# Kernel tuning notes

Measured on AMD Instinct MI355X. Metric: run time of the kernel, lower is better.

Reference implementation:

```python
import jax, jax.numpy as jnp
import numpy as np

D_MODEL = 1024
N_HEADS = 16
D_HEAD = D_MODEL // N_HEADS  # 64
SCALE = 1.0 / float(np.sqrt(D_HEAD))


def setup_inputs() -> dict:
    key = jax.random.key(0)
    kx, kq, kk, kv, ko = jax.random.split(key, 5)
    B, L = 1, 4096
    x = jax.random.normal(kx, (B, L, D_MODEL), dtype=jnp.float32)
    init = 0.02  # small init so softmax isn't saturated
    Wq = jax.random.normal(kq, (D_MODEL, D_MODEL), dtype=jnp.float32) * init
    Wk = jax.random.normal(kk, (D_MODEL, D_MODEL), dtype=jnp.float32) * init
    Wv = jax.random.normal(kv, (D_MODEL, D_MODEL), dtype=jnp.float32) * init
    Wo = jax.random.normal(ko, (D_MODEL, D_MODEL), dtype=jnp.float32) * init
    return {"x": x, "Wq": Wq, "Wk": Wk, "Wv": Wv, "Wo": Wo}


def reference(x, Wq, Wk, Wv, Wo):
    # x: [B, L, d_model]; torch Linear (no bias): y = x @ W.T
    B, L, _ = x.shape

    def split_heads(t):  # [B, L, d_model] -> [B, H, L, Dh]
        return t.reshape(B, L, N_HEADS, D_HEAD).transpose(0, 2, 1, 3)

    q = split_heads(x @ Wq.T)
    k = split_heads(x @ Wk.T)
    v = split_heads(x @ Wv.T)

    # Full (non-flash) attention: explicit [B, H, L, L] scores (causal=False, eval dropout=0)
    scores = jnp.einsum("bhld,bhmd->bhlm", q, k) * SCALE
    attn = jax.nn.softmax(scores, axis=-1)
    out = jnp.einsum("bhlm,bhmd->bhld", attn, v)

    out = out.transpose(0, 2, 1, 3).reshape(B, L, D_MODEL)
    return out @ Wo.T
```

## Files before the change

### kernel.cpp

```cpp
#include <hip/hip_runtime.h>

typedef _Float16 f16_t;
typedef __fp16 fp16x2 __attribute__((ext_vector_type(2)));
typedef _Float16 f16x2 __attribute__((ext_vector_type(2)));
typedef _Float16 f16x4 __attribute__((ext_vector_type(4)));
typedef _Float16 f16x8 __attribute__((ext_vector_type(8)));
typedef float f32x4 __attribute__((ext_vector_type(4)));

#define D_MODEL 1024
#define LSEQ 4096
#define NH 16
#define DH 64
#define QSCALE 0.18033688011112042f

#define GLDS16(g, l)                                                     \
    __builtin_amdgcn_global_load_lds(                                    \
        (const __attribute__((address_space(1))) void*)(g),              \
        (__attribute__((address_space(3))) void*)(l), 16, 0, 0)

#define WAIT_VM(n) asm volatile("s_waitcnt vmcnt(" #n ")" ::: "memory")

__global__ __launch_bounds__(256) void cvt_all(const float* __restrict__ x,
                                               const float* __restrict__ w0,
                                               const float* __restrict__ w1,
                                               const float* __restrict__ w2,
                                               const float* __restrict__ w3,
                                               f16_t* __restrict__ xb,
                                               f16_t* __restrict__ wq) {
    const int id = blockIdx.x;
    const float* src;
    f16_t* dst;
    float scale = 1.f;
    int i;
    if (id < 4096) {
        src = x; dst = xb;
        i = (id * 256 + threadIdx.x) * 4;
    } else {
        const int r = id - 4096;
        const int q = r >> 10;
        src = (q == 0) ? w0 : (q == 1) ? w1 : (q == 2) ? w2 : w3;
        if (q == 0) scale = QSCALE;
        dst = wq + (size_t)q * (D_MODEL * D_MODEL);
        i = ((r & 1023) * 256 + threadIdx.x) * 4;
    }
    float4 v = *(const float4*)&src[i];
    alignas(8) f16_t o4[4] = {(f16_t)(v.x * scale), (f16_t)(v.y * scale),
                              (f16_t)(v.z * scale), (f16_t)(v.w * scale)};
    *(uint2*)&dst[i] = *(const uint2*)o4;
}

__global__ __launch_bounds__(256, 3) void gemm_f16(const f16_t* __restrict__ A,
                                                   const f16_t* __restrict__ B,
                                                   void* __restrict__ Cout,
                                                   f16_t* __restrict__ v4out,
                                                   int M, int N, int K, int mode) {
    __shared__ alignas(16) f16_t sm[24576];

    const int tid  = threadIdx.x;
    const int wave = tid >> 6;
    const int lane = tid & 63;
    const int quad = lane >> 4;
    const int l16  = lane & 15;
    const int wm = (wave & 1) * 64;
    const int wn = (wave >> 1) * 64;

    const int gx  = gridDim.x;
    const int gy  = gridDim.y;
    const int lid = blockIdx.y * gx + blockIdx.x;
    const int xcd = lid & 7;
    const int sub = lid >> 3;
    const int bm  = (xcd * (gx >> 3) + sub / gy) * 128;
    const int bn  = (sub % gy) * 128;

    f32x4 acc[4][4] = {};
    const int nk = K / 32;

    auto stage = [&](int kt, int b) {
        const int c0 = wave * 2;
        GLDS16(&A[(size_t)(bm + c0 * 16 + l16) * K + kt * 32 + quad * 8],
               &sm[b * 4096 + c0 * 512]);
        GLDS16(&A[(size_t)(bm + (c0 + 1) * 16 + l16) * K + kt * 32 + quad * 8],
               &sm[b * 4096 + (c0 + 1) * 512]);
        GLDS16(&B[(size_t)(bn + c0 * 16 + l16) * K + kt * 32 + quad * 8],
               &sm[12288 + b * 4096 + c0 * 512]);
        GLDS16(&B[(size_t)(bn + (c0 + 1) * 16 + l16) * K + kt * 32 + quad * 8],
               &sm[12288 + b * 4096 + (c0 + 1) * 512]);
    };

    stage(0, 0);
    stage(1, 1);
    for (int kt = 0; kt < nk; ++kt) {
        const int cb = kt % 3;
        if (kt < nk - 1) WAIT_VM(4);
        else             WAIT_VM(0);
        __syncthreads();
        if (kt + 2 < nk) stage(kt + 2, (kt + 2) % 3);

        f16x8 af[4], bfr[4];
#pragma unroll
        for (int mt = 0; mt < 4; ++mt)
            af[mt] = *(const f16x8*)&sm[cb * 4096 + ((wm >> 4) + mt) * 512 + lane * 8];
#pragma unroll
        for (int nt = 0; nt < 4; ++nt)
            bfr[nt] = *(const f16x8*)&sm[12288 + cb * 4096 + ((wn >> 4) + nt) * 512 + lane * 8];
#pragma unroll
        for (int mt = 0; mt < 4; ++mt)
#pragma unroll
            for (int nt = 0; nt < 4; ++nt)
                acc[mt][nt] = __builtin_amdgcn_mfma_f32_16x16x32_f16(
                    bfr[nt], af[mt], acc[mt][nt], 0, 0, 0);
    }

    const bool isV = (mode == 0) && (bn >= 2 * D_MODEL);
    if (!isV) {
#pragma unroll
        for (int mt = 0; mt < 4; ++mt)
#pragma unroll
            for (int nt = 0; nt < 4; ++nt) {
                int row = bm + wm + mt * 16 + l16;
                int col = bn + wn + nt * 16 + quad * 4;
                if (mode == 0) {
                    f16x4 p = {(f16_t)acc[mt][nt][0], (f16_t)acc[mt][nt][1],
                               (f16_t)acc[mt][nt][2], (f16_t)acc[mt][nt][3]};
                    *(f16x4*)&((f16_t*)Cout)[((size_t)(col >> 6) * M + row) * 64 +
                                             (col & 63)] = p;
                } else {
                    *(f32x4*)&((float*)Cout)[(size_t)row * N + col] = acc[mt][nt];
                }
            }
    } else {
        __syncthreads();
#pragma unroll
        for (int mt = 0; mt < 4; ++mt)
#pragma unroll
            for (int nt = 0; nt < 4; ++nt) {
                f16x4 p = {(f16_t)acc[mt][nt][0], (f16_t)acc[mt][nt][1],
                           (f16_t)acc[mt][nt][2], (f16_t)acc[mt][nt][3]};
                *(f16x4*)&sm[(wm + mt * 16 + l16) * 136 + wn + nt * 16 + quad * 4] = p;
            }
        __syncthreads();
        const int hh = wave >> 1, lt = wave & 1;
        const int head = ((bn - 2 * D_MODEL) >> 6) + hh;
        const int ltg  = (bm >> 6) + lt;
        const int g = lane >> 4, l16f = lane & 15;
        f16_t* dst = v4out + (size_t)head * (LSEQ * DH) + (size_t)ltg * 4096;
#pragma unroll
        for (int c8 = 0; c8 < 8; ++c8) {
            const int mtp = c8 >> 2, dt = c8 & 3;
            alignas(16) f16_t buf[8];
#pragma unroll
            for (int j = 0; j < 8; ++j) {
                int key = lt * 64 + mtp * 32 + (j < 4 ? 4 * g + j : 16 + 4 * g + (j - 4));
                buf[j] = sm[key * 136 + hh * 64 + dt * 16 + l16f];
            }
            *(uint4*)&dst[c8 * 512 + lane * 8] = *(const uint4*)buf;
        }
    }
}

__global__ __launch_bounds__(512, 2) void gemm_wo(const f16_t* __restrict__ A,
                                                  const f16_t* __restrict__ B,
                                                  float* __restrict__ outF) {
    __shared__ alignas(16) f16_t sm[24576];

    const int tid  = threadIdx.x;
    const int wave = tid >> 6;
    const int lane = tid & 63;
    const int quad = lane >> 4;
    const int l16  = lane & 15;
    const int wm = (wave & 1) * 64;
    const int wn = (wave >> 1) * 32;
    const int bm = blockIdx.x * 128;
    const int bn = blockIdx.y * 128;
    const int K = D_MODEL;

    f32x4 acc[4][2] = {};
    const int nk = K / 32;

    auto stage = [&](int kt, int b) {
        f16_t* base = sm + b * 8192;
        GLDS16(&A[(size_t)(bm + wave * 16 + l16) * K + kt * 32 + quad * 8],
               &base[wave * 512]);
        GLDS16(&B[(size_t)(bn + wave * 16 + l16) * K + kt * 32 + quad * 8],
               &base[4096 + wave * 512]);
    };

    stage(0, 0);
    stage(1, 1);
    for (int kt = 0; kt < nk; ++kt) {
        const int cb = kt % 3;
        if (kt < nk - 1) WAIT_VM(2);
        else             WAIT_VM(0);
        __syncthreads();
        if (kt + 2 < nk) stage(kt + 2, (kt + 2) % 3);

        f16x8 af[4], bfr[2];
#pragma unroll
        for (int mt = 0; mt < 4; ++mt)
            af[mt] = *(const f16x8*)&sm[cb * 8192 + ((wm >> 4) + mt) * 512 + lane * 8];
#pragma unroll
        for (int nt = 0; nt < 2; ++nt)
            bfr[nt] = *(const f16x8*)&sm[cb * 8192 + 4096 + ((wn >> 4) + nt) * 512 + lane * 8];
#pragma unroll
        for (int mt = 0; mt < 4; ++mt)
#pragma unroll
            for (int nt = 0; nt < 2; ++nt)
                acc[mt][nt] = __builtin_amdgcn_mfma_f32_16x16x32_f16(
                    bfr[nt], af[mt], acc[mt][nt], 0, 0, 0);
    }

#pragma unroll
    for (int mt = 0; mt < 4; ++mt)
#pragma unroll
        for (int nt = 0; nt < 2; ++nt) {
            int row = bm + wm + mt * 16 + l16;
            int col = bn + wn + nt * 16 + quad * 4;
            *(f32x4*)&outF[(size_t)row * D_MODEL + col] = acc[mt][nt];
        }
}

__global__ __launch_bounds__(512, 4) void attn_kernel(const f16_t* __restrict__ qh,
                                                      const f16_t* __restrict__ kh,
                                                      const f16_t* __restrict__ v4,
                                                      f16_t* __restrict__ ao) {
    __shared__ alignas(16) f16_t smem[32768];
    __shared__ alignas(16) float lscr[8 * 64];
    f16_t* KsB = smem;
    f16_t* VsB = smem + 16384;

    const int tid  = threadIdx.x;
    const int wave = tid >> 6;
    const int lane = tid & 63;
    const int quad = lane >> 4;
    const int l16  = lane & 15;
    const int wq   = wave & 3;
    const int kha  = wave >> 2;

    const int id = blockIdx.x;
    const int head = id & 15;
    const int qrow0 = (id >> 4) * 128 + wq * 32;

    const f16_t* Q  = qh + (size_t)head * LSEQ * DH;
    const f16_t* K  = kh + (size_t)head * LSEQ * DH;
    const f16_t* V4 = v4 + (size_t)head * (LSEQ * DH);

    f16x8 qf[2][2];
#pragma unroll
    for (int qt = 0; qt < 2; ++qt)
#pragma unroll
        for (int kc = 0; kc < 2; ++kc)
            qf[qt][kc] = *(const f16x8*)
                &Q[(size_t)(qrow0 + qt * 16 + l16) * DH + kc * 32 + quad * 8];

    f32x4 o[4][2] = {};
    float lp[2] = {0.f, 0.f};

    auto stage = [&](int kt, int b) {
        f16_t* ks = KsB + (kha * 2 + b) * 4096;
        f16_t* vs = VsB + (kha * 2 + b) * 4096;
        const int ktg = kha * 32 + kt;
#pragma unroll
        for (int jj = 0; jj < 2; ++jj) {
            const int j = wq * 2 + jj;
            GLDS16(&K[(size_t)(ktg * 64 + wq * 16 + l16) * DH + jj * 32 + quad * 8],
                   &ks[j * 512]);
            GLDS16(&V4[(size_t)ktg * 4096 + wq * 1024 + jj * 512 + lane * 8],
                   &vs[wq * 1024 + jj * 512]);
        }
    };

    const int NT = LSEQ / 2 / 64;
    stage(0, 0);
    for (int kt = 0; kt < NT; ++kt) {
        const int cb = kt & 1;
        WAIT_VM(0);
        __syncthreads();
        if (kt + 1 < NT) stage(kt + 1, cb ^ 1);

        const f16_t* ks = KsB + (kha * 2 + cb) * 4096;
        const f16_t* vs = VsB + (kha * 2 + cb) * 4096;

        f32x4 sA[2][2] = {};
        {
            f16x8 kfA[4];
#pragma unroll
            for (int c = 0; c < 4; ++c)
                kfA[c] = *(const f16x8*)&ks[c * 512 + lane * 8];
#pragma unroll
            for (int h = 0; h < 2; ++h)
#pragma unroll
                for (int qt = 0; qt < 2; ++qt) {
                    sA[h][qt] = __builtin_amdgcn_mfma_f32_16x16x32_f16(
                        kfA[h * 2 + 0], qf[qt][0], sA[h][qt], 0, 0, 0);
                    sA[h][qt] = __builtin_amdgcn_mfma_f32_16x16x32_f16(
                        kfA[h * 2 + 1], qf[qt][1], sA[h][qt], 0, 0, 0);
                }
        }
        f32x4 sB[2][2] = {};
        {
            f16x8 kfB[4];
#pragma unroll
            for (int c = 0; c < 4; ++c)
                kfB[c] = *(const f16x8*)&ks[(4 + c) * 512 + lane * 8];
#pragma unroll
            for (int h = 0; h < 2; ++h)
#pragma unroll
                for (int qt = 0; qt < 2; ++qt) {
                    sB[h][qt] = __builtin_amdgcn_mfma_f32_16x16x32_f16(
                        kfB[h * 2 + 0], qf[qt][0], sB[h][qt], 0, 0, 0);
                    sB[h][qt] = __builtin_amdgcn_mfma_f32_16x16x32_f16(
                        kfB[h * 2 + 1], qf[qt][1], sB[h][qt], 0, 0, 0);
                }
        }

#pragma unroll
        for (int mtp = 0; mtp < 2; ++mtp) {
            f32x4 (*s)[2] = (mtp == 0) ? sA : sB;

            f16x8 vfd[4];
#pragma unroll
            for (int dt = 0; dt < 4; ++dt)
                vfd[dt] = *(const f16x8*)&vs[(mtp * 4 + dt) * 512 + lane * 8];

#pragma unroll
            for (int qt = 0; qt < 2; ++qt) {
                float e0 = __builtin_amdgcn_exp2f(s[0][qt][0]);
                float e1 = __builtin_amdgcn_exp2f(s[0][qt][1]);
                float e2 = __builtin_amdgcn_exp2f(s[0][qt][2]);
                float e3 = __builtin_amdgcn_exp2f(s[0][qt][3]);
                float e4 = __builtin_amdgcn_exp2f(s[1][qt][0]);
                float e5 = __builtin_amdgcn_exp2f(s[1][qt][1]);
                float e6 = __builtin_amdgcn_exp2f(s[1][qt][2]);
                float e7 = __builtin_amdgcn_exp2f(s[1][qt][3]);
                lp[qt] += ((e0 + e1) + (e2 + e3)) + ((e4 + e5) + (e6 + e7));
                fp16x2 p01 = __builtin_amdgcn_cvt_pkrtz(e0, e1);
                fp16x2 p23 = __builtin_amdgcn_cvt_pkrtz(e2, e3);
                fp16x2 p45 = __builtin_amdgcn_cvt_pkrtz(e4, e5);
                fp16x2 p67 = __builtin_amdgcn_cvt_pkrtz(e6, e7);
                f16x8 p = {__builtin_bit_cast(f16x2, p01)[0],
                           __builtin_bit_cast(f16x2, p01)[1],
                           __builtin_bit_cast(f16x2, p23)[0],
                           __builtin_bit_cast(f16x2, p23)[1],
                           __builtin_bit_cast(f16x2, p45)[0],
                           __builtin_bit_cast(f16x2, p45)[1],
                           __builtin_bit_cast(f16x2, p67)[0],
                           __builtin_bit_cast(f16x2, p67)[1]};
#pragma unroll
                for (int dt = 0; dt < 4; ++dt)
                    o[dt][qt] = __builtin_amdgcn_mfma_f32_16x16x32_f16(
                        vfd[dt], p, o[dt][qt], 0, 0, 0);
            }
        }
    }

    __syncthreads();
    float* scr = (float*)smem;
    if (wave >= 4) {
#pragma unroll
        for (int dt = 0; dt < 4; ++dt)
#pragma unroll
            for (int qt = 0; qt < 2; ++qt)
                *(f32x4*)&scr[(((wave - 4) * 8 + dt * 2 + qt) * 64 + lane) * 4] =
                    o[dt][qt];
#pragma unroll
        for (int qt = 0; qt < 2; ++qt)
            lscr[((wave - 4) * 2 + qt) * 64 + lane] = lp[qt];
    }
    __syncthreads();
    if (wave < 4) {
#pragma unroll
        for (int dt = 0; dt < 4; ++dt)
#pragma unroll
            for (int qt = 0; qt < 2; ++qt)
                o[dt][qt] += *(const f32x4*)
                    &scr[((wave * 8 + dt * 2 + qt) * 64 + lane) * 4];
#pragma unroll
        for (int qt = 0; qt < 2; ++qt) {
            float t = lp[qt] + lscr[(wave * 2 + qt) * 64 + lane];
            t += __shfl_xor(t, 16, 64);
            t += __shfl_xor(t, 32, 64);
            lp[qt] = 1.f / t;
        }
#pragma unroll
        for (int dt = 0; dt < 4; ++dt)
#pragma unroll
            for (int qt = 0; qt < 2; ++qt) {
                f16x4 ov = {(f16_t)(o[dt][qt][0] * lp[qt]),
                            (f16_t)(o[dt][qt][1] * lp[qt]),
                            (f16_t)(o[dt][qt][2] * lp[qt]),
                            (f16_t)(o[dt][qt][3] * lp[qt])};
                int qrow = qrow0 + qt * 16 + l16;
                *(f16x4*)&ao[(size_t)qrow * D_MODEL + head * 64 + dt * 16 +
                             quad * 4] = ov;
            }
    }
}

extern "C" void kernel_launch(void* const* d_in, const int* in_sizes, int n_in,
                              void* d_out, int out_size, void* d_ws, size_t ws_size,
                              hipStream_t stream) {
    const float* x  = (const float*)d_in[0];
    const float* Wq = (const float*)d_in[1];
    const float* Wk = (const float*)d_in[2];
    const float* Wv = (const float*)d_in[3];
    const float* Wo = (const float*)d_in[4];

    f16_t* xb = (f16_t*)d_ws;
    f16_t* wq = xb + (size_t)LSEQ * D_MODEL;
    f16_t* wo = wq + (size_t)3 * D_MODEL * D_MODEL;
    f16_t* qh = wo + (size_t)D_MODEL * D_MODEL;
    f16_t* kh = qh + (size_t)LSEQ * D_MODEL;
    f16_t* vh = kh + (size_t)LSEQ * D_MODEL;
    f16_t* v4 = vh + (size_t)LSEQ * D_MODEL;
    f16_t* ao = v4 + (size_t)LSEQ * D_MODEL;

    cvt_all<<<4096 + 4 * 1024, 256, 0, stream>>>(x, Wq, Wk, Wv, Wo, xb, wq);

    gemm_f16<<<dim3(LSEQ / 128, 3 * D_MODEL / 128), 256, 0, stream>>>(
        xb, wq, qh, v4, LSEQ, 3 * D_MODEL, D_MODEL, 0);

    attn_kernel<<<dim3((LSEQ / 128) * NH), 512, 0, stream>>>(qh, kh, v4, ao);

    gemm_wo<<<dim3(LSEQ / 128, D_MODEL / 128), 512, 0, stream>>>(
        ao, wo, (float*)d_out);
}
```

Baseline: 230.0 us.

## Fuse attention and output projection into one kernel with per-row-group counters

After: 266.8 us. 16.0% more time.

```diff
diff --git a/kernel.cpp b/kernel.cpp
--- a/kernel.cpp
+++ b/kernel.cpp
@@ -26,8 +26,10 @@
                                                const float* __restrict__ w2,
                                                const float* __restrict__ w3,
                                                f16_t* __restrict__ xb,
-                                               f16_t* __restrict__ wq) {
+                                               f16_t* __restrict__ wq,
+                                               unsigned int* __restrict__ cnt) {
     const int id = blockIdx.x;
+    if (id == 0 && threadIdx.x < 32) cnt[threadIdx.x] = 0;
     const float* src;
     f16_t* dst;
     float scale = 1.f;
@@ -158,240 +160,250 @@
     }
 }
 
-__global__ __launch_bounds__(512, 2) void gemm_wo(const f16_t* __restrict__ A,
-                                                  const f16_t* __restrict__ B,
-                                                  float* __restrict__ outF) {
-    __shared__ alignas(16) f16_t sm[24576];
+__global__ __launch_bounds__(512, 4) void attn_wo(
+        const f16_t* __restrict__ qh, const f16_t* __restrict__ kh,
+        const f16_t* __restrict__ v4, f16_t* __restrict__ ao,
+        const f16_t* __restrict__ wo, float* __restrict__ outF,
+        unsigned int* __restrict__ cnt) {
+    __shared__ alignas(16) f16_t smem[32768];
+    __shared__ alignas(16) float lscr[8 * 64];
 
     const int tid  = threadIdx.x;
     const int wave = tid >> 6;
     const int lane = tid & 63;
     const int quad = lane >> 4;
     const int l16  = lane & 15;
-    const int wm = (wave & 1) * 64;
-    const int wn = (wave >> 1) * 32;
-    const int bm = blockIdx.x * 128;
-    const int bn = blockIdx.y * 128;
-    const int K = D_MODEL;
-
-    f32x4 acc[4][2] = {};
-    const int nk = K / 32;
-
-    auto stage = [&](int kt, int b) {
-        f16_t* base = sm + b * 8192;
-        GLDS16(&A[(size_t)(bm + wave * 16 + l16) * K + kt * 32 + quad * 8],
-               &base[wave * 512]);
-        GLDS16(&B[(size_t)(bn + wave * 16 + l16) * K + kt * 32 + quad * 8],
-               &base[4096 + wave * 512]);
-    };
-
-    stage(0, 0);
-    stage(1, 1);
-    for (int kt = 0; kt < nk; ++kt) {
-        const int cb = kt % 3;
-        if (kt < nk - 1) WAIT_VM(2);
-        else             WAIT_VM(0);
-        __syncthreads();
-        if (kt + 2 < nk) stage(kt + 2, (kt + 2) % 3);
-
-        f16x8 af[4], bfr[2];
+
+    if (blockIdx.x < 512) {
+        f16_t* KsB = smem;
+        f16_t* VsB = smem + 16384;
+        const int wq  = wave & 3;
+        const int kha = wave >> 2;
+
+        const int id = blockIdx.x;
+        const int head = id & 15;
+        const int qrow0 = (id >> 4) * 128 + wq * 32;
+
+        const f16_t* Q  = qh + (size_t)head * LSEQ * DH;
+        const f16_t* K  = kh + (size_t)head * LSEQ * DH;
+        const f16_t* V4 = v4 + (size_t)head * (LSEQ * DH);
+
+        f16x8 qf[2][2];
+#pragma unroll
+        for (int qt = 0; qt < 2; ++qt)
+#pragma unroll
+            for (int kc = 0; kc < 2; ++kc)
+                qf[qt][kc] = *(const f16x8*)
+                    &Q[(size_t)(qrow0 + qt * 16 + l16) * DH + kc * 32 + quad * 8];
+
+        f32x4 o[4][2] = {};
+        float lp[2] = {0.f, 0.f};
+
+        auto stage = [&](int kt, int b) {
+            f16_t* ks = KsB + (kha * 2 + b) * 4096;
+            f16_t* vs = VsB + (kha * 2 + b) * 4096;
+            const int ktg = kha * 32 + kt;
+#pragma unroll
+            for (int jj = 0; jj < 2; ++jj) {
+                const int j = wq * 2 + jj;
+                GLDS16(&K[(size_t)(ktg * 64 + wq * 16 + l16) * DH + jj * 32 + quad * 8],
+                       &ks[j * 512]);
+                GLDS16(&V4[(size_t)ktg * 4096 + wq * 1024 + jj * 512 + lane * 8],
+                       &vs[wq * 1024 + jj * 512]);
+            }
+        };
+
+        const int NT = LSEQ / 2 / 64;
+        stage(0, 0);
+        for (int kt = 0; kt < NT; ++kt) {
+            const int cb = kt & 1;
+            WAIT_VM(0);
+            __syncthreads();
+            if (kt + 1 < NT) stage(kt + 1, cb ^ 1);
+
+            const f16_t* ks = KsB + (kha * 2 + cb) * 4096;
+            const f16_t* vs = VsB + (kha * 2 + cb) * 4096;
+
+            f32x4 sA[2][2] = {};
+            {
+                f16x8 kfA[4];
+#pragma unroll
+                for (int c = 0; c < 4; ++c)
+                    kfA[c] = *(const f16x8*)&ks[c * 512 + lane * 8];
+#pragma unroll
+                for (int h = 0; h < 2; ++h)
+#pragma unroll
+                    for (int qt = 0; qt < 2; ++qt) {
+                        sA[h][qt] = __builtin_amdgcn_mfma_f32_16x16x32_f16(
+                            kfA[h * 2 + 0], qf[qt][0], sA[h][qt], 0, 0, 0);
+                        sA[h][qt] = __builtin_amdgcn_mfma_f32_16x16x32_f16(
+                            kfA[h * 2 + 1], qf[qt][1], sA[h][qt], 0, 0, 0);
+                    }
+            }
+            f32x4 sB[2][2] = {};
+            {
+                f16x8 kfB[4];
+#pragma unroll
+                for (int c = 0; c < 4; ++c)
+                    kfB[c] = *(const f16x8*)&ks[(4 + c) * 512 + lane * 8];
+#pragma unroll
+                for (int h = 0; h < 2; ++h)
+#pragma unroll
+                    for (int qt = 0; qt < 2; ++qt) {
+                        sB[h][qt] = __builtin_amdgcn_mfma_f32_16x16x32_f16(
+                            kfB[h * 2 + 0], qf[qt][0], sB[h][qt], 0, 0, 0);
+                        sB[h][qt] = __builtin_amdgcn_mfma_f32_16x16x32_f16(
+                            kfB[h * 2 + 1], qf[qt][1], sB[h][qt], 0, 0, 0);
+                    }
+            }
+
+#pragma unroll
+            for (int mtp = 0; mtp < 2; ++mtp) {
+                f32x4 (*s)[2] = (mtp == 0) ? sA : sB;
+
+                f16x8 vfd[4];
+#pragma unroll
+                for (int dt = 0; dt < 4; ++dt)
+                    vfd[dt] = *(const f16x8*)&vs[(mtp * 4 + dt) * 512 + lane * 8];
+
+#pragma unroll
+                for (int qt = 0; qt < 2; ++qt) {
+                    float e0 = __builtin_amdgcn_exp2f(s[0][qt][0]);
+                    float e1 = __builtin_amdgcn_exp2f(s[0][qt][1]);
+                    float e2 = __builtin_amdgcn_exp2f(s[0][qt][2]);
+                    float e3 = __builtin_amdgcn_exp2f(s[0][qt][3]);
+                    float e4 = __builtin_amdgcn_exp2f(s[1][qt][0]);
+                    float e5 = __builtin_amdgcn_exp2f(s[1][qt][1]);
+                    float e6 = __builtin_amdgcn_exp2f(s[1][qt][2]);
+                    float e7 = __builtin_amdgcn_exp2f(s[1][qt][3]);
+                    lp[qt] += ((e0 + e1) + (e2 + e3)) + ((e4 + e5) + (e6 + e7));
+                    fp16x2 p01 = __builtin_amdgcn_cvt_pkrtz(e0, e1);
+                    fp16x2 p23 = __builtin_amdgcn_cvt_pkrtz(e2, e3);
+                    fp16x2 p45 = __builtin_amdgcn_cvt_pkrtz(e4, e5);
+                    fp16x2 p67 = __builtin_amdgcn_cvt_pkrtz(e6, e7);
+                    f16x8 p = {__builtin_bit_cast(f16x2, p01)[0],
+                               __builtin_bit_cast(f16x2, p01)[1],
+                               __builtin_bit_cast(f16x2, p23)[0],
+                               __builtin_bit_cast(f16x2, p23)[1],
+                               __builtin_bit_cast(f16x2, p45)[0],
+                               __builtin_bit_cast(f16x2, p45)[1],
+                               __builtin_bit_cast(f16x2, p67)[0],
+                               __builtin_bit_cast(f16x2, p67)[1]};
+#pragma unroll
+                    for (int dt = 0; dt < 4; ++dt)
+                        o[dt][qt] = __builtin_amdgcn_mfma_f32_16x16x32_f16(
+                            vfd[dt], p, o[dt][qt], 0, 0, 0);
+                }
+            }
+        }
+
+        __syncthreads();
+        float* scr = (float*)smem;
+        if (wave >= 4) {
+#pragma unroll
+            for (int dt = 0; dt < 4; ++dt)
+#pragma unroll
+                for (int qt = 0; qt < 2; ++qt)
+                    *(f32x4*)&scr[(((wave - 4) * 8 + dt * 2 + qt) * 64 + lane) * 4] =
+                        o[dt][qt];
+#pragma unroll
+            for (int qt = 0; qt < 2; ++qt)
+                lscr[((wave - 4) * 2 + qt) * 64 + lane] = lp[qt];
+        }
+        __syncthreads();
+        if (wave < 4) {
+#pragma unroll
+            for (int dt = 0; dt < 4; ++dt)
+#pragma unroll
+                for (int qt = 0; qt < 2; ++qt)
+                    o[dt][qt] += *(const f32x4*)
+                        &scr[((wave * 8 + dt * 2 + qt) * 64 + lane) * 4];
+#pragma unroll
+            for (int qt = 0; qt < 2; ++qt) {
+                float t = lp[qt] + lscr[(wave * 2 + qt) * 64 + lane];
+                t += __shfl_xor(t, 16, 64);
+                t += __shfl_xor(t, 32, 64);
+                lp[qt] = 1.f / t;
+            }
+#pragma unroll
+            for (int dt = 0; dt < 4; ++dt)
+#pragma unroll
+                for (int qt = 0; qt < 2; ++qt) {
+                    f16x4 ov = {(f16_t)(o[dt][qt][0] * lp[qt]),
+                                (f16_t)(o[dt][qt][1] * lp[qt]),
+                                (f16_t)(o[dt][qt][2] * lp[qt]),
+                                (f16_t)(o[dt][qt][3] * lp[qt])};
+                    int qrow = qrow0 + qt * 16 + l16;
+                    *(f16x4*)&ao[(size_t)qrow * D_MODEL + head * 64 + dt * 16 +
+                                 quad * 4] = ov;
+                }
+        }
+
+        __syncthreads();
+        if (tid == 0) {
+            __threadfence();
+            atomicAdd(&cnt[id >> 4], 1u);
+        }
+    } else {
+        const int wid = blockIdx.x - 512;
+        const int rg  = wid >> 3;
+        const int bm  = rg * 128;
+        const int bn  = (wid & 7) * 128;
+
+        if (tid == 0) {
+            while (atomicAdd(&cnt[rg], 0u) < 16u)
+                __builtin_amdgcn_s_sleep(16);
+            __threadfence();
+        }
+        __syncthreads();
+
+        f16_t* sm = smem;
+        const int wm = (wave & 1) * 64;
+        const int wn = (wave >> 1) * 32;
+        const int K = D_MODEL;
+
+        f32x4 acc[4][2] = {};
+        const int nk = K / 32;
+
+        auto stageW = [&](int kt, int b) {
+            f16_t* base = sm + b * 8192;
+            GLDS16(&ao[(size_t)(bm + wave * 16 + l16) * K + kt * 32 + quad * 8],
+                   &base[wave * 512]);
+            GLDS16(&wo[(size_t)(bn + wave * 16 + l16) * K + kt * 32 + quad * 8],
+                   &base[4096 + wave * 512]);
+        };
+
+        stageW(0, 0);
+        stageW(1, 1);
+        for (int kt = 0; kt < nk; ++kt) {
+            const int cb = kt % 3;
+            if (kt < nk - 1) WAIT_VM(2);
+            else             WAIT_VM(0);
+            __syncthreads();
+            if (kt + 2 < nk) stageW(kt + 2, (kt + 2) % 3);
+
+            f16x8 af[4], bfr[2];
+#pragma unroll
+            for (int mt = 0; mt < 4; ++mt)
+                af[mt] = *(const f16x8*)&sm[cb * 8192 + ((wm >> 4) + mt) * 512 + lane * 8];
+#pragma unroll
+            for (int nt = 0; nt < 2; ++nt)
+                bfr[nt] = *(const f16x8*)&sm[cb * 8192 + 4096 + ((wn >> 4) + nt) * 512 + lane * 8];
+#pragma unroll
+            for (int mt = 0; mt < 4; ++mt)
+#pragma unroll
+                for (int nt = 0; nt < 2; ++nt)
+                    acc[mt][nt] = __builtin_amdgcn_mfma_f32_16x16x32_f16(
+                        bfr[nt], af[mt], acc[mt][nt], 0, 0, 0);
+        }
+
 #pragma unroll
         for (int mt = 0; mt < 4; ++mt)
-            af[mt] = *(const f16x8*)&sm[cb * 8192 + ((wm >> 4) + mt) * 512 + lane * 8];
-#pragma unroll
-        for (int nt = 0; nt < 2; ++nt)
-            bfr[nt] = *(const f16x8*)&sm[cb * 8192 + 4096 + ((wn >> 4) + nt) * 512 + lane * 8];
-#pragma unroll
-        for (int mt = 0; mt < 4; ++mt)
-#pragma unroll
-            for (int nt = 0; nt < 2; ++nt)
-                acc[mt][nt] = __builtin_amdgcn_mfma_f32_16x16x32_f16(
-                    bfr[nt], af[mt], acc[mt][nt], 0, 0, 0);
-    }
-
-#pragma unroll
-    for (int mt = 0; mt < 4; ++mt)
-#pragma unroll
-        for (int nt = 0; nt < 2; ++nt) {
-            int row = bm + wm + mt * 16 + l16;
-            int col = bn + wn + nt * 16 + quad * 4;
-            *(f32x4*)&outF[(size_t)row * D_MODEL + col] = acc[mt][nt];
-        }
-}
-
-__global__ __launch_bounds__(512, 4) void attn_kernel(const f16_t* __restrict__ qh,
-                                                      const f16_t* __restrict__ kh,
-                                                      const f16_t* __restrict__ v4,
-                                                      f16_t* __restrict__ ao) {
-    __shared__ alignas(16) f16_t smem[32768];
-    __shared__ alignas(16) float lscr[8 * 64];
-    f16_t* KsB = smem;
-    f16_t* VsB = smem + 16384;
-
-    const int tid  = threadIdx.x;
-    const int wave = tid >> 6;
-    const int lane = tid & 63;
-    const int quad = lane >> 4;
-    const int l16  = lane & 15;
-    const int wq   = wave & 3;
-    const int kha  = wave >> 2;
-
-    const int id = blockIdx.x;
-    const int head = id & 15;
-    const int qrow0 = (id >> 4) * 128 + wq * 32;
-
-    const f16_t* Q  = qh + (size_t)head * LSEQ * DH;
-    const f16_t* K  = kh + (size_t)head * LSEQ * DH;
-    const f16_t* V4 = v4 + (size_t)head * (LSEQ * DH);
-
-    f16x8 qf[2][2];
-#pragma unroll
-    for (int qt = 0; qt < 2; ++qt)
-#pragma unroll
-        for (int kc = 0; kc < 2; ++kc)
-            qf[qt][kc] = *(const f16x8*)
-                &Q[(size_t)(qrow0 + qt * 16 + l16) * DH + kc * 32 + quad * 8];
-
-    f32x4 o[4][2] = {};
-    float lp[2] = {0.f, 0.f};
-
-    auto stage = [&](int kt, int b) {
-        f16_t* ks = KsB + (kha * 2 + b) * 4096;
-        f16_t* vs = VsB + (kha * 2 + b) * 4096;
-        const int ktg = kha * 32 + kt;
-#pragma unroll
-        for (int jj = 0; jj < 2; ++jj) {
-            const int j = wq * 2 + jj;
-            GLDS16(&K[(size_t)(ktg * 64 + wq * 16 + l16) * DH + jj * 32 + quad * 8],
-                   &ks[j * 512]);
-            GLDS16(&V4[(size_t)ktg * 4096 + wq * 1024 + jj * 512 + lane * 8],
-                   &vs[wq * 1024 + jj * 512]);
-        }
-    };
-
-    const int NT = LSEQ / 2 / 64;
-    stage(0, 0);
-    for (int kt = 0; kt < NT; ++kt) {
-        const int cb = kt & 1;
-        WAIT_VM(0);
-        __syncthreads();
-        if (kt + 1 < NT) stage(kt + 1, cb ^ 1);
-
-        const f16_t* ks = KsB + (kha * 2 + cb) * 4096;
-        const f16_t* vs = VsB + (kha * 2 + cb) * 4096;
-
-        f32x4 sA[2][2] = {};
-        {
-            f16x8 kfA[4];
-#pragma unroll
-            for (int c = 0; c < 4; ++c)
-                kfA[c] = *(const f16x8*)&ks[c * 512 + lane * 8];
-#pragma unroll
-            for (int h = 0; h < 2; ++h)
-#pragma unroll
-                for (int qt = 0; qt < 2; ++qt) {
-                    sA[h][qt] = __builtin_amdgcn_mfma_f32_16x16x32_f16(
-                        kfA[h * 2 + 0], qf[qt][0], sA[h][qt], 0, 0, 0);
-                    sA[h][qt] = __builtin_amdgcn_mfma_f32_16x16x32_f16(
-                        kfA[h * 2 + 1], qf[qt][1], sA[h][qt], 0, 0, 0);
-                }
-        }
-        f32x4 sB[2][2] = {};
-        {
-            f16x8 kfB[4];
-#pragma unroll
-            for (int c = 0; c < 4; ++c)
-                kfB[c] = *(const f16x8*)&ks[(4 + c) * 512 + lane * 8];
-#pragma unroll
-            for (int h = 0; h < 2; ++h)
-#pragma unroll
-                for (int qt = 0; qt < 2; ++qt) {
-                    sB[h][qt] = __builtin_amdgcn_mfma_f32_16x16x32_f16(
-                        kfB[h * 2 + 0], qf[qt][0], sB[h][qt], 0, 0, 0);
-                    sB[h][qt] = __builtin_amdgcn_mfma_f32_16x16x32_f16(
-                        kfB[h * 2 + 1], qf[qt][1], sB[h][qt], 0, 0, 0);
-                }
-        }
-
-#pragma unroll
-        for (int mtp = 0; mtp < 2; ++mtp) {
-            f32x4 (*s)[2] = (mtp == 0) ? sA : sB;
-
-            f16x8 vfd[4];
-#pragma unroll
-            for (int dt = 0; dt < 4; ++dt)
-                vfd[dt] = *(const f16x8*)&vs[(mtp * 4 + dt) * 512 + lane * 8];
-
-#pragma unroll
-            for (int qt = 0; qt < 2; ++qt) {
-                float e0 = __builtin_amdgcn_exp2f(s[0][qt][0]);
-                float e1 = __builtin_amdgcn_exp2f(s[0][qt][1]);
-                float e2 = __builtin_amdgcn_exp2f(s[0][qt][2]);
-                float e3 = __builtin_amdgcn_exp2f(s[0][qt][3]);
-                float e4 = __builtin_amdgcn_exp2f(s[1][qt][0]);
-                float e5 = __builtin_amdgcn_exp2f(s[1][qt][1]);
-                float e6 = __builtin_amdgcn_exp2f(s[1][qt][2]);
-                float e7 = __builtin_amdgcn_exp2f(s[1][qt][3]);
-                lp[qt] += ((e0 + e1) + (e2 + e3)) + ((e4 + e5) + (e6 + e7));
-                fp16x2 p01 = __builtin_amdgcn_cvt_pkrtz(e0, e1);
-                fp16x2 p23 = __builtin_amdgcn_cvt_pkrtz(e2, e3);
-                fp16x2 p45 = __builtin_amdgcn_cvt_pkrtz(e4, e5);
-                fp16x2 p67 = __builtin_amdgcn_cvt_pkrtz(e6, e7);
-                f16x8 p = {__builtin_bit_cast(f16x2, p01)[0],
-                           __builtin_bit_cast(f16x2, p01)[1],
-                           __builtin_bit_cast(f16x2, p23)[0],
-                           __builtin_bit_cast(f16x2, p23)[1],
-                           __builtin_bit_cast(f16x2, p45)[0],
-                           __builtin_bit_cast(f16x2, p45)[1],
-                           __builtin_bit_cast(f16x2, p67)[0],
-                           __builtin_bit_cast(f16x2, p67)[1]};
-#pragma unroll
-                for (int dt = 0; dt < 4; ++dt)
-                    o[dt][qt] = __builtin_amdgcn_mfma_f32_16x16x32_f16(
-                        vfd[dt], p, o[dt][qt], 0, 0, 0);
-            }
-        }
-    }
-
-    __syncthreads();
-    float* scr = (float*)smem;
-    if (wave >= 4) {
-#pragma unroll
-        for (int dt = 0; dt < 4; ++dt)
-#pragma unroll
-            for (int qt = 0; qt < 2; ++qt)
-                *(f32x4*)&scr[(((wave - 4) * 8 + dt * 2 + qt) * 64 + lane) * 4] =
-                    o[dt][qt];
-#pragma unroll
-        for (int qt = 0; qt < 2; ++qt)
-            lscr[((wave - 4) * 2 + qt) * 64 + lane] = lp[qt];
-    }
-    __syncthreads();
-    if (wave < 4) {
-#pragma unroll
-        for (int dt = 0; dt < 4; ++dt)
-#pragma unroll
-            for (int qt = 0; qt < 2; ++qt)
-                o[dt][qt] += *(const f32x4*)
-                    &scr[((wave * 8 + dt * 2 + qt) * 64 + lane) * 4];
-#pragma unroll
-        for (int qt = 0; qt < 2; ++qt) {
-            float t = lp[qt] + lscr[(wave * 2 + qt) * 64 + lane];
-            t += __shfl_xor(t, 16, 64);
-            t += __shfl_xor(t, 32, 64);
-            lp[qt] = 1.f / t;
-        }
-#pragma unroll
-        for (int dt = 0; dt < 4; ++dt)
-#pragma unroll
-            for (int qt = 0; qt < 2; ++qt) {
-                f16x4 ov = {(f16_t)(o[dt][qt][0] * lp[qt]),
-                            (f16_t)(o[dt][qt][1] * lp[qt]),
-                            (f16_t)(o[dt][qt][2] * lp[qt]),
-                            (f16_t)(o[dt][qt][3] * lp[qt])};
-                int qrow = qrow0 + qt * 16 + l16;
-                *(f16x4*)&ao[(size_t)qrow * D_MODEL + head * 64 + dt * 16 +
-                             quad * 4] = ov;
+#pragma unroll
+            for (int nt = 0; nt < 2; ++nt) {
+                int row = bm + wm + mt * 16 + l16;
+                int col = bn + wn + nt * 16 + quad * 4;
+                *(f32x4*)&outF[(size_t)row * D_MODEL + col] = acc[mt][nt];
             }
     }
 }
@@ -413,14 +425,13 @@
     f16_t* vh = kh + (size_t)LSEQ * D_MODEL;
     f16_t* v4 = vh + (size_t)LSEQ * D_MODEL;
     f16_t* ao = v4 + (size_t)LSEQ * D_MODEL;
-
-    cvt_all<<<4096 + 4 * 1024, 256, 0, stream>>>(x, Wq, Wk, Wv, Wo, xb, wq);
+    unsigned int* cnt = (unsigned int*)(ao + (size_t)LSEQ * D_MODEL);
+
+    cvt_all<<<4096 + 4 * 1024, 256, 0, stream>>>(x, Wq, Wk, Wv, Wo, xb, wq, cnt);
 
     gemm_f16<<<dim3(LSEQ / 128, 3 * D_MODEL / 128), 256, 0, stream>>>(
         xb, wq, qh, v4, LSEQ, 3 * D_MODEL, D_MODEL, 0);
 
-    attn_kernel<<<dim3((LSEQ / 128) * NH), 512, 0, stream>>>(qh, kh, v4, ao);
-
-    gemm_wo<<<dim3(LSEQ / 128, D_MODEL / 128), 512, 0, stream>>>(
-        ao, wo, (float*)d_out);
+    attn_wo<<<dim3(512 + 256), 512, 0, stream>>>(
+        qh, kh, v4, ao, wo, (float*)d_out, cnt);
 }
```
